# Performance work log

Hardware: AMD Instinct MI355X
Metric: run time of the kernel (lower is better)

## Reference

```python
import jax, jax.numpy as jnp
import numpy as np

B, L, E, H = 1024, 50, 256, 256
NEG = -1e9          # stands in for -inf masked_fill (exp(NEG) == 0 in fp32)
C_EXPL = 10.0       # tanh_exploration for the pointer head
N_GLIMPSES = 1


def setup_inputs() -> dict:
    key = jax.random.key(0)
    ks = jax.random.split(key, 20)
    s = 1.0 / np.sqrt(H).astype(np.float32)
    return {
        "decoder_input": jax.random.normal(ks[0], (B, E), jnp.float32),
        "embedded_inputs": jax.random.normal(ks[1], (L, B, E), jnp.float32),
        "h0": jax.random.normal(ks[2], (B, H), jnp.float32),
        "c0": jax.random.normal(ks[3], (B, H), jnp.float32),
        "context": jax.random.normal(ks[4], (L, B, H), jnp.float32),
        "init_mask": jnp.zeros((B, L), dtype=bool),
        "lstm_Wih": jax.random.normal(ks[5], (4 * H, E), jnp.float32) * s,
        "lstm_Whh": jax.random.normal(ks[6], (4 * H, H), jnp.float32) * s,
        "lstm_bih": jax.random.normal(ks[7], (4 * H,), jnp.float32) * s,
        "lstm_bhh": jax.random.normal(ks[8], (4 * H,), jnp.float32) * s,
        "gl_Wq": jax.random.normal(ks[9], (H, H), jnp.float32) * s,
        "gl_bq": jax.random.normal(ks[10], (H,), jnp.float32) * s,
        "gl_Wref": jax.random.normal(ks[11], (H, H), jnp.float32) * s,
        "gl_bref": jax.random.normal(ks[12], (H,), jnp.float32) * s,
        "gl_v": jax.random.uniform(ks[13], (H,), jnp.float32, -s, s),
        "pt_Wq": jax.random.normal(ks[14], (H, H), jnp.float32) * s,
        "pt_bq": jax.random.normal(ks[15], (H, H // H * H,)[:1] and (H,), jnp.float32) * s,
        "pt_Wref": jax.random.normal(ks[16], (H, H), jnp.float32) * s,
        "pt_bref": jax.random.normal(ks[17], (H,), jnp.float32) * s,
        "pt_v": jax.random.uniform(ks[18], (H,), jnp.float32, -s, s),
    }


def _attention(Wq, bq, Wref, bref, v, query, context, use_tanh):
    # context: [L,B,H], query: [B,H]
    e = jnp.einsum('lbh,oh->lbo', context, Wref) + bref      # conv1d(k=1) proj of ref
    q = query @ Wq.T + bq                                    # [B,H]
    u = jnp.einsum('lbh,h->bl', jnp.tanh(q[None, :, :] + e), v)
    if use_tanh:
        u = C_EXPL * jnp.tanh(u)
    return e, u


def _lstm_cell(x, h, c, Wih, Whh, bih, bhh):
    g = x @ Wih.T + bih + h @ Whh.T + bhh
    i, f, gg, o = jnp.split(g, 4, axis=1)   # torch LSTMCell gate order: i,f,g,o
    c2 = jax.nn.sigmoid(f) * c + jax.nn.sigmoid(i) * jnp.tanh(gg)
    h2 = jax.nn.sigmoid(o) * jnp.tanh(c2)
    return h2, c2


def reference(decoder_input, embedded_inputs, h0, c0, context, init_mask,
              lstm_Wih, lstm_Whh, lstm_bih, lstm_bhh,
              gl_Wq, gl_bq, gl_Wref, gl_bref, gl_v,
              pt_Wq, pt_bq, pt_Wref, pt_bref, pt_v):
    batch_idx = jnp.arange(B)

    def step(carry, t):
        h, c, mask, idxs, dec_in = carry
        # update_mask(mask, selected), skipped at step 0 (prev_idxs is None)
        safe = jnp.maximum(idxs, 0)
        m2 = mask.at[batch_idx, safe].set(True)
        m2 = m2.at[:, -1].set(jnp.where(m2.all(axis=1), False, m2[:, -1]))
        logit_mask = jnp.where(t == 0, mask, m2)
        # LSTM cell
        hy, cy = _lstm_cell(dec_in, h, c, lstm_Wih, lstm_Whh, lstm_bih, lstm_bhh)
        g_l = hy
        # glimpse attention(s) (mask_glimpses=True)
        for _ in range(N_GLIMPSES):
            e, gl = _attention(gl_Wq, gl_bq, gl_Wref, gl_bref, gl_v, g_l, context, False)
            gl = jnp.where(logit_mask, NEG, gl)
            g_l = jnp.einsum('lbh,bl->bh', e, jax.nn.softmax(gl, axis=1))
        # pointer attention (mask_logits=True)
        _, logits = _attention(pt_Wq, pt_bq, pt_Wref, pt_bref, pt_v, g_l, context, True)
        logits = jnp.where(logit_mask, NEG, logits)
        log_p = jax.nn.log_softmax(logits, axis=1)          # [B,L]
        new_idxs = jax.lax.stop_gradient(jnp.argmax(log_p, axis=1))  # greedy decode (detached)
        new_dec_in = embedded_inputs[new_idxs, batch_idx]   # gather next input [B,E]
        return (hy, cy, logit_mask, new_idxs, new_dec_in), (log_p, new_idxs)

    init = (h0, c0, init_mask, jnp.full((B,), -1, dtype=jnp.int32), decoder_input)
    _, (log_ps, sels) = jax.lax.scan(step, init, jnp.arange(L))
    # stack along time dim 1, as torch.stack(outputs, 1)
    return jnp.transpose(log_ps, (1, 0, 2)), jnp.transpose(sels, (1, 0))
```

## Files before the change

### kernel.cpp

```cpp
#include <hip/hip_runtime.h>
#include <math.h>

#define Bsz 1024
#define Lsz 50
#define Esz 256
#define Hsz 256
#define NEGV (-1e9f)

__global__ void init_kernel(const float* __restrict__ dec0,
                            float* __restrict__ dec,
                            int* __restrict__ mask)
{
    int i = blockIdx.x * 256 + threadIdx.x;
    dec[i] = dec0[i];
    if (i < Bsz * Lsz) mask[i] = 0;
}

__global__ void pack_wq(const float* __restrict__ WqGl, const float* __restrict__ WqPt,
                        float* __restrict__ WqGlP, float* __restrict__ WqPtP)
{
    int k = blockIdx.x;
    int n = threadIdx.x;
    const float* src = blockIdx.y ? WqPt : WqGl;
    float*       dst = blockIdx.y ? WqPtP : WqGlP;
    dst[((size_t)(k >> 2) * 256 + n) * 4 + (k & 3)] = src[(size_t)n * 256 + k];
}

__global__ __launch_bounds__(256) void eproj_kernel(
    const float* __restrict__ A,
    const float* __restrict__ Wgl, const float* __restrict__ bgl, float* __restrict__ Egl,
    const float* __restrict__ Wpt, const float* __restrict__ bpt, float* __restrict__ Ept)
{
    __shared__ __align__(16) float As[16][68];
    __shared__ __align__(16) float Bs[16][68];
    const int tid = threadIdx.x;
    const int tx = tid & 15, ty = tid >> 4;
    const int ml = tid >> 2;
    const int kb = (tid & 3) << 2;

    const int x = blockIdx.x;
    const int xcd = x & 7;
    const int j = x >> 3;
    const int mt = xcd * 100 + (j >> 3);
    const int sel = (j >> 2) & 1;
    const int nt = j & 3;
    const float* W    = sel ? Wpt : Wgl;
    const float* bias = sel ? bpt : bgl;
    float*       Eo   = sel ? Ept : Egl;
    const int m0 = mt * 64, n0 = nt * 64;

    float4 a4 = *(const float4*)(A + (size_t)(m0 + ml) * 256 + kb);
    float4 b4 = *(const float4*)(W + (size_t)(n0 + ml) * 256 + kb);

    float acc[4][4] = {};
    for (int k0 = 0; k0 < 256; k0 += 16) {
        As[kb+0][ml] = a4.x; As[kb+1][ml] = a4.y; As[kb+2][ml] = a4.z; As[kb+3][ml] = a4.w;
        Bs[kb+0][ml] = b4.x; Bs[kb+1][ml] = b4.y; Bs[kb+2][ml] = b4.z; Bs[kb+3][ml] = b4.w;
        __syncthreads();
        int k1 = k0 + 16;
        if (k1 < 256) {
            a4 = *(const float4*)(A + (size_t)(m0 + ml) * 256 + k1 + kb);
            b4 = *(const float4*)(W + (size_t)(n0 + ml) * 256 + k1 + kb);
        }
#pragma unroll
        for (int kk = 0; kk < 16; kk++) {
            float4 av = *(const float4*)(&As[kk][ty << 2]);
            float4 bv = *(const float4*)(&Bs[kk][tx << 2]);
            float a_[4] = {av.x, av.y, av.z, av.w};
            float b_[4] = {bv.x, bv.y, bv.z, bv.w};
#pragma unroll
            for (int i = 0; i < 4; i++)
#pragma unroll
                for (int j2 = 0; j2 < 4; j2++) acc[i][j2] = fmaf(a_[i], b_[j2], acc[i][j2]);
        }
        __syncthreads();
    }
#pragma unroll
    for (int i = 0; i < 4; i++) {
        int m = m0 + (ty << 2) + i;
        int bb = m & (Bsz - 1);
        int ll = m >> 10;
#pragma unroll
        for (int j2 = 0; j2 < 4; j2++) {
            int n = n0 + (tx << 2) + j2;
            Eo[(size_t)bb * Lsz * Hsz + (size_t)ll * Hsz + n] = acc[i][j2] + bias[n];
        }
    }
}

__global__ __launch_bounds__(256) void lstm_fused(
    const float* __restrict__ dec, const float* __restrict__ hprev,
    const float* __restrict__ cin,
    const float* __restrict__ Wih, const float* __restrict__ Whh,
    const float* __restrict__ bih, const float* __restrict__ bhh,
    float* __restrict__ hout, float* __restrict__ cout)
{
    __shared__ __align__(16) float As[16][36];
    __shared__ __align__(16) float Bs[16][68];
    const int tid = threadIdx.x;
    const int tx = tid & 15, ty = tid >> 4;
    const int mlA = tid >> 3;
    const int kbA = (tid & 7) << 1;
    const int mlB = tid >> 2;
    const int kbB = (tid & 3) << 2;
    const int m0 = blockIdx.x * 32;
    const int hh0 = blockIdx.y * 16;
    const int wrow = ((mlB >> 4) << 8) + hh0 + (mlB & 15);
    const int pcol = ((mlB & 15) << 2) + (mlB >> 4);

    float2 a2 = *(const float2*)(dec + (size_t)(m0 + mlA) * 256 + kbA);
    float4 b4 = *(const float4*)(Wih + (size_t)wrow * 256 + kbB);

    float acc[2][4] = {};
    for (int k0 = 0; k0 < 512; k0 += 16) {
        As[kbA+0][mlA] = a2.x; As[kbA+1][mlA] = a2.y;
        Bs[kbB+0][pcol] = b4.x; Bs[kbB+1][pcol] = b4.y;
        Bs[kbB+2][pcol] = b4.z; Bs[kbB+3][pcol] = b4.w;
        __syncthreads();
        int k1 = k0 + 16;
        if (k1 < 512) {
            const float* Ap = (k1 < 256) ? dec : hprev;
            const float* Wp = (k1 < 256) ? Wih : Whh;
            int kk0 = k1 & 255;
            a2 = *(const float2*)(Ap + (size_t)(m0 + mlA) * 256 + kk0 + kbA);
            b4 = *(const float4*)(Wp + (size_t)wrow * 256 + kk0 + kbB);
        }
#pragma unroll
        for (int kk = 0; kk < 16; kk++) {
            float2 av = *(const float2*)(&As[kk][ty << 1]);
            float4 bv = *(const float4*)(&Bs[kk][tx << 2]);
            acc[0][0] = fmaf(av.x, bv.x, acc[0][0]);
            acc[0][1] = fmaf(av.x, bv.y, acc[0][1]);
            acc[0][2] = fmaf(av.x, bv.z, acc[0][2]);
            acc[0][3] = fmaf(av.x, bv.w, acc[0][3]);
            acc[1][0] = fmaf(av.y, bv.x, acc[1][0]);
            acc[1][1] = fmaf(av.y, bv.y, acc[1][1]);
            acc[1][2] = fmaf(av.y, bv.z, acc[1][2]);
            acc[1][3] = fmaf(av.y, bv.w, acc[1][3]);
        }
        __syncthreads();
    }

    const int hh = hh0 + tx;
    const float bi0 = bih[hh]       + bhh[hh];
    const float bf  = bih[256 + hh] + bhh[256 + hh];
    const float bg  = bih[512 + hh] + bhh[512 + hh];
    const float bo  = bih[768 + hh] + bhh[768 + hh];
#pragma unroll
    for (int i = 0; i < 2; i++) {
        int m = m0 + (ty << 1) + i;
        float gi = acc[i][0] + bi0;
        float gf = acc[i][1] + bf;
        float gc = acc[i][2] + bg;
        float go = acc[i][3] + bo;
        float ii = 1.0f / (1.0f + expf(-gi));
        float ff = 1.0f / (1.0f + expf(-gf));
        float oo = 1.0f / (1.0f + expf(-go));
        float c2 = ff * cin[(size_t)m * 256 + hh] + ii * tanhf(gc);
        hout[(size_t)m * 256 + hh] = oo * tanhf(c2);
        cout[(size_t)m * 256 + hh] = c2;
    }
}

__global__ __launch_bounds__(256) void attn_row(
    const float* __restrict__ h,
    const float* __restrict__ WqGlP, const float* __restrict__ glbq,
    const float* __restrict__ e_gl, const float* __restrict__ glv,
    const float* __restrict__ WqPtP, const float* __restrict__ ptbq,
    const float* __restrict__ e_pt, const float* __restrict__ ptv,
    int* __restrict__ mask, float* __restrict__ out, int t,
    float* __restrict__ dec, const float* __restrict__ emb)
{
    __shared__ __align__(16) float h_s[256];
    __shared__ __align__(16) float q_s[256];
    __shared__ __align__(16) float g_s[256];
    __shared__ float u_s[64];
    __shared__ float p_s[64];
    __shared__ int sel_s;

    const int tid = threadIdx.x;
    const int lane = tid & 63, wave = tid >> 6;
    const int b = blockIdx.x;

    h_s[tid] = h[(size_t)b * 256 + tid];
    __syncthreads();

    {
        float q = glbq[tid];
        const float4* Wp = (const float4*)WqGlP;
#pragma unroll 8
        for (int k4 = 0; k4 < 64; k4++) {
            float4 w  = Wp[(size_t)k4 * 256 + tid];
            float4 hv = ((const float4*)h_s)[k4];
            q = fmaf(hv.x, w.x, q);
            q = fmaf(hv.y, w.y, q);
            q = fmaf(hv.z, w.z, q);
            q = fmaf(hv.w, w.w, q);
        }
        q_s[tid] = q;
    }
    __syncthreads();

    const float* ebg = e_gl + (size_t)b * Lsz * 256;
    {
        const float4 q4 = ((const float4*)q_s)[lane];
        const float4 v4 = ((const float4*)glv)[lane];
#pragma unroll
        for (int lp = 0; lp < 13; lp++) {
            const int l = lp * 4 + wave;
            float x = 0.0f;
            if (l < Lsz) {
                float4 e4 = *(const float4*)(ebg + (size_t)l * 256 + (lane << 2));
                x  = v4.x * tanhf(q4.x + e4.x);
                x += v4.y * tanhf(q4.y + e4.y);
                x += v4.z * tanhf(q4.z + e4.z);
                x += v4.w * tanhf(q4.w + e4.w);
            }
#pragma unroll
            for (int o = 32; o > 0; o >>= 1) x += __shfl_xor(x, o, 64);
            if (lane == 0 && l < Lsz) u_s[l] = x;
        }
    }
    __syncthreads();

    if (wave == 0) {
        const int l = lane;
        const int ml = (l < Lsz) ? mask[b * Lsz + l] : 0;
        float logit = (l < Lsz) ? (ml ? NEGV : u_s[l]) : -1e30f;
        float m = logit;
#pragma unroll
        for (int o = 32; o > 0; o >>= 1) m = fmaxf(m, __shfl_xor(m, o, 64));
        float ex = (l < Lsz) ? expf(logit - m) : 0.0f;
        float den = ex;
#pragma unroll
        for (int o = 32; o > 0; o >>= 1) den += __shfl_xor(den, o, 64);
        if (l < Lsz) p_s[l] = ex / den;
    }
    __syncthreads();

    {
        float acc = 0.0f;
        const float* ebh = ebg + tid;
#pragma unroll
        for (int l = 0; l < Lsz; l++)
            acc = fmaf(p_s[l], ebh[(size_t)l * 256], acc);
        g_s[tid] = acc;
    }
    __syncthreads();

    {
        float p = ptbq[tid];
        const float4* Wp = (const float4*)WqPtP;
#pragma unroll 8
        for (int k4 = 0; k4 < 64; k4++) {
            float4 w  = Wp[(size_t)k4 * 256 + tid];
            float4 gv = ((const float4*)g_s)[k4];
            p = fmaf(gv.x, w.x, p);
            p = fmaf(gv.y, w.y, p);
            p = fmaf(gv.z, w.z, p);
            p = fmaf(gv.w, w.w, p);
        }
        q_s[tid] = p;
    }
    __syncthreads();

    const float* ebp = e_pt + (size_t)b * Lsz * 256;
    {
        const float4 q4 = ((const float4*)q_s)[lane];
        const float4 v4 = ((const float4*)ptv)[lane];
#pragma unroll
        for (int lp = 0; lp < 13; lp++) {
            const int l = lp * 4 + wave;
            float x = 0.0f;
            if (l < Lsz) {
                float4 e4 = *(const float4*)(ebp + (size_t)l * 256 + (lane << 2));
                x  = v4.x * tanhf(q4.x + e4.x);
                x += v4.y * tanhf(q4.y + e4.y);
                x += v4.z * tanhf(q4.z + e4.z);
                x += v4.w * tanhf(q4.w + e4.w);
            }
#pragma unroll
            for (int o = 32; o > 0; o >>= 1) x += __shfl_xor(x, o, 64);
            if (lane == 0 && l < Lsz) u_s[l] = x;
        }
    }
    __syncthreads();

    if (wave == 0) {
        const int l = lane;
        const int ml = (l < Lsz) ? mask[b * Lsz + l] : 0;
        float logit;
        if (l < Lsz) {
            float u = u_s[l];
            logit = 10.0f * tanhf(u);
            if (ml) logit = NEGV;
        } else logit = -1e30f;

        float m = logit;
#pragma unroll
        for (int o = 32; o > 0; o >>= 1) m = fmaxf(m, __shfl_xor(m, o, 64));
        float ex = (l < Lsz) ? expf(logit - m) : 0.0f;
        float den = ex;
#pragma unroll
        for (int o = 32; o > 0; o >>= 1) den += __shfl_xor(den, o, 64);

        float av = logit; int ai = (l < Lsz) ? l : 63;
#pragma unroll
        for (int o = 32; o > 0; o >>= 1) {
            float ov = __shfl_xor(av, o, 64);
            int   oi = __shfl_xor(ai, o, 64);
            if (ov > av || (ov == av && oi < ai)) { av = ov; ai = oi; }
        }
        const float lse = m + logf(den);
        if (l < Lsz)
            out[(size_t)b * Lsz * Lsz + (size_t)t * Lsz + l] = logit - lse;
        if (l == 0) {
            out[(size_t)Bsz * Lsz * Lsz + (size_t)b * Lsz + t] = (float)ai;
            sel_s = ai;
        }
        int newm = ml | (l == ai);
        unsigned long long bal = __ballot(l >= Lsz ? 1 : newm);
        int all = (bal == 0xFFFFFFFFFFFFFFFFull);
        if (l < Lsz) mask[b * Lsz + l] = (all && l == Lsz - 1) ? 0 : newm;
    }
    __syncthreads();

    {
        const int s = sel_s;
        dec[(size_t)b * 256 + tid] = emb[(size_t)s * Bsz * 256 + (size_t)b * 256 + tid];
    }
}

extern "C" void kernel_launch(void* const* d_in, const int* in_sizes, int n_in,
                              void* d_out, int out_size, void* d_ws, size_t ws_size,
                              hipStream_t stream) {
    const float* decoder_input = (const float*)d_in[0];
    const float* emb           = (const float*)d_in[1];
    const float* h0            = (const float*)d_in[2];
    const float* c0            = (const float*)d_in[3];
    const float* context       = (const float*)d_in[4];
    const float* Wih    = (const float*)d_in[6];
    const float* Whh    = (const float*)d_in[7];
    const float* bih    = (const float*)d_in[8];
    const float* bhh    = (const float*)d_in[9];
    const float* glWq   = (const float*)d_in[10];
    const float* glbq   = (const float*)d_in[11];
    const float* glWref = (const float*)d_in[12];
    const float* glbref = (const float*)d_in[13];
    const float* glv    = (const float*)d_in[14];
    const float* ptWq   = (const float*)d_in[15];
    const float* ptbq   = (const float*)d_in[16];
    const float* ptWref = (const float*)d_in[17];
    const float* ptbref = (const float*)d_in[18];
    const float* ptv    = (const float*)d_in[19];

    float* out = (float*)d_out;

    float* ws    = (float*)d_ws;
    float* e_gl  = ws;
    float* e_pt  = e_gl + (size_t)Bsz * Lsz * Hsz;
    float* WqGlP = e_pt + (size_t)Bsz * Lsz * Hsz;
    float* WqPtP = WqGlP + (size_t)Hsz * Hsz;
    float* hb0   = WqPtP + (size_t)Hsz * Hsz;
    float* hb1   = hb0 + (size_t)Bsz * Hsz;
    float* cb0   = hb1 + (size_t)Bsz * Hsz;
    float* cb1   = cb0 + (size_t)Bsz * Hsz;
    float* dec   = cb1 + (size_t)Bsz * Hsz;
    int*   mask  = (int*)(dec + (size_t)Bsz * Esz);

    float* hbuf[2] = {hb0, hb1};
    float* cbuf[2] = {cb0, cb1};

    init_kernel<<<dim3(Bsz), dim3(256), 0, stream>>>(decoder_input, dec, mask);
    pack_wq<<<dim3(256, 2), dim3(256), 0, stream>>>(glWq, ptWq, WqGlP, WqPtP);

    eproj_kernel<<<dim3(6400), dim3(256), 0, stream>>>(
        context, glWref, glbref, e_gl, ptWref, ptbref, e_pt);

    for (int t = 0; t < Lsz; t++) {
        const float* hin = (t == 0) ? h0 : hbuf[(t + 1) & 1];
        const float* cin = (t == 0) ? c0 : cbuf[(t + 1) & 1];
        float* hout = hbuf[t & 1];
        float* cout = cbuf[t & 1];

        lstm_fused<<<dim3(32, 16), dim3(256), 0, stream>>>(
            dec, hin, cin, Wih, Whh, bih, bhh, hout, cout);

        attn_row<<<dim3(Bsz), dim3(256), 0, stream>>>(
            hout, WqGlP, glbq, e_gl, glv, WqPtP, ptbq, e_pt, ptv,
            mask, out, t, dec, emb);
    }
}
```

Baseline: 4.141 ms.

## Fuse decode loop into one cooperative persistent kernel with group counters

```diff
diff --git a/kernel.cpp b/kernel.cpp
--- a/kernel.cpp
+++ b/kernel.cpp
@@ -9,11 +9,13 @@
 
 __global__ void init_kernel(const float* __restrict__ dec0,
                             float* __restrict__ dec,
-                            int* __restrict__ mask)
+                            int* __restrict__ mask,
+                            int* __restrict__ cnts)
 {
     int i = blockIdx.x * 256 + threadIdx.x;
     dec[i] = dec0[i];
     if (i < Bsz * Lsz) mask[i] = 0;
+    if (i < 64) cnts[i] = 0;
 }
 
 __global__ void pack_wq(const float* __restrict__ WqGl, const float* __restrict__ WqPt,
@@ -328,6 +330,288 @@
     {
         const int s = sel_s;
         dec[(size_t)b * 256 + tid] = emb[(size_t)s * Bsz * 256 + (size_t)b * 256 + tid];
+    }
+}
+
+__global__ __launch_bounds__(256, 4) void decode_loop(
+    const float* __restrict__ h0, const float* __restrict__ c0,
+    const float* __restrict__ Wih, const float* __restrict__ Whh,
+    const float* __restrict__ bih, const float* __restrict__ bhh,
+    const float* __restrict__ WqGlP, const float* __restrict__ glbq,
+    const float* __restrict__ e_gl, const float* __restrict__ glv,
+    const float* __restrict__ WqPtP, const float* __restrict__ ptbq,
+    const float* __restrict__ e_pt, const float* __restrict__ ptv,
+    const float* __restrict__ emb,
+    float* __restrict__ hb0, float* __restrict__ hb1,
+    float* __restrict__ dec, float* __restrict__ out,
+    int* __restrict__ hcnt, int* __restrict__ deccnt)
+{
+    __shared__ __align__(16) float As[16][36];
+    __shared__ __align__(16) float Bs[16][68];
+    __shared__ __align__(16) float h_s[256];
+    __shared__ __align__(16) float q_s[256];
+    __shared__ __align__(16) float g_s[256];
+    __shared__ float u_s[64];
+    __shared__ float p_s[64];
+    __shared__ int  mask_s[64];
+    __shared__ int  sel_s;
+
+    const int tid  = threadIdx.x;
+    const int bid  = blockIdx.x;
+    const int g    = bid >> 5;
+    const int lane = tid & 63, wave = tid >> 6;
+    const bool is_lstm = (bid & 1) == 0;
+
+    const int lstm_id = bid >> 1;
+    const int tx = tid & 15, ty = tid >> 4;
+    const int mlA = tid >> 3, kbA = (tid & 7) << 1;
+    const int mlB = tid >> 2, kbB = (tid & 3) << 2;
+    const int m0  = (lstm_id >> 4) * 32;
+    const int hh0 = (lstm_id & 15) * 16;
+    const int wrow = ((mlB >> 4) << 8) + hh0 + (mlB & 15);
+    const int pcol = ((mlB & 15) << 2) + (mlB >> 4);
+    const int hh = hh0 + tx;
+
+    float creg[2] = {0.f, 0.f};
+    float bi0 = 0.f, bfv = 0.f, bgv = 0.f, bov = 0.f;
+    if (is_lstm) {
+        bi0 = bih[hh]       + bhh[hh];
+        bfv = bih[256 + hh] + bhh[256 + hh];
+        bgv = bih[512 + hh] + bhh[512 + hh];
+        bov = bih[768 + hh] + bhh[768 + hh];
+#pragma unroll
+        for (int i = 0; i < 2; i++) {
+            int m = m0 + (ty << 1) + i;
+            creg[i] = c0[(size_t)m * 256 + hh];
+        }
+    }
+    if (tid < 64) mask_s[tid] = 0;
+
+    const float* ebg = e_gl + (size_t)bid * Lsz * 256;
+    const float* ebp = e_pt + (size_t)bid * Lsz * 256;
+
+    for (int t = 0; t < Lsz; t++) {
+        float* hout = (t & 1) ? hb1 : hb0;
+
+        if (is_lstm) {
+            const float* hin = (t == 0) ? h0 : ((t & 1) ? hb0 : hb1);
+            if (t > 0) {
+                if (tid == 0) {
+                    while (__hip_atomic_load(&deccnt[g], __ATOMIC_RELAXED,
+                                             __HIP_MEMORY_SCOPE_AGENT) < 32 * t)
+                        __builtin_amdgcn_s_sleep(2);
+                    __threadfence();
+                }
+                __syncthreads();
+            }
+
+            float2 a2 = *(const float2*)(dec + (size_t)(m0 + mlA) * 256 + kbA);
+            float4 b4 = *(const float4*)(Wih + (size_t)wrow * 256 + kbB);
+
+            float acc[2][4] = {};
+            for (int k0 = 0; k0 < 512; k0 += 16) {
+                As[kbA+0][mlA] = a2.x; As[kbA+1][mlA] = a2.y;
+                Bs[kbB+0][pcol] = b4.x; Bs[kbB+1][pcol] = b4.y;
+                Bs[kbB+2][pcol] = b4.z; Bs[kbB+3][pcol] = b4.w;
+                __syncthreads();
+                int k1 = k0 + 16;
+                if (k1 < 512) {
+                    const float* Ap = (k1 < 256) ? dec : hin;
+                    const float* Wp = (k1 < 256) ? Wih : Whh;
+                    int kk0 = k1 & 255;
+                    a2 = *(const float2*)(Ap + (size_t)(m0 + mlA) * 256 + kk0 + kbA);
+                    b4 = *(const float4*)(Wp + (size_t)wrow * 256 + kk0 + kbB);
+                }
+#pragma unroll
+                for (int kk = 0; kk < 16; kk++) {
+                    float2 av = *(const float2*)(&As[kk][ty << 1]);
+                    float4 bv = *(const float4*)(&Bs[kk][tx << 2]);
+                    acc[0][0] = fmaf(av.x, bv.x, acc[0][0]);
+                    acc[0][1] = fmaf(av.x, bv.y, acc[0][1]);
+                    acc[0][2] = fmaf(av.x, bv.z, acc[0][2]);
+                    acc[0][3] = fmaf(av.x, bv.w, acc[0][3]);
+                    acc[1][0] = fmaf(av.y, bv.x, acc[1][0]);
+                    acc[1][1] = fmaf(av.y, bv.y, acc[1][1]);
+                    acc[1][2] = fmaf(av.y, bv.z, acc[1][2]);
+                    acc[1][3] = fmaf(av.y, bv.w, acc[1][3]);
+                }
+                __syncthreads();
+            }
+
+#pragma unroll
+            for (int i = 0; i < 2; i++) {
+                int m = m0 + (ty << 1) + i;
+                float gi = acc[i][0] + bi0;
+                float gf = acc[i][1] + bfv;
+                float gc = acc[i][2] + bgv;
+                float go = acc[i][3] + bov;
+                float ii = 1.0f / (1.0f + expf(-gi));
+                float ff = 1.0f / (1.0f + expf(-gf));
+                float oo = 1.0f / (1.0f + expf(-go));
+                float c2 = ff * creg[i] + ii * tanhf(gc);
+                creg[i] = c2;
+                hout[(size_t)m * 256 + hh] = oo * tanhf(c2);
+            }
+            __syncthreads();
+            if (tid == 0) { __threadfence(); atomicAdd(&hcnt[g], 1); }
+        }
+
+        if (tid == 0) {
+            while (__hip_atomic_load(&hcnt[g], __ATOMIC_RELAXED,
+                                     __HIP_MEMORY_SCOPE_AGENT) < 16 * (t + 1))
+                __builtin_amdgcn_s_sleep(2);
+            __threadfence();
+        }
+        __syncthreads();
+
+        h_s[tid] = hout[(size_t)bid * 256 + tid];
+        __syncthreads();
+
+        {
+            float q = glbq[tid];
+            const float4* Wp = (const float4*)WqGlP;
+#pragma unroll 8
+            for (int k4 = 0; k4 < 64; k4++) {
+                float4 w  = Wp[(size_t)k4 * 256 + tid];
+                float4 hv = ((const float4*)h_s)[k4];
+                q = fmaf(hv.x, w.x, q);
+                q = fmaf(hv.y, w.y, q);
+                q = fmaf(hv.z, w.z, q);
+                q = fmaf(hv.w, w.w, q);
+            }
+            q_s[tid] = q;
+        }
+        __syncthreads();
+
+        {
+            const float4 q4 = ((const float4*)q_s)[lane];
+            const float4 v4 = ((const float4*)glv)[lane];
+#pragma unroll
+            for (int lp = 0; lp < 13; lp++) {
+                const int l = lp * 4 + wave;
+                float x = 0.0f;
+                if (l < Lsz) {
+                    float4 e4 = *(const float4*)(ebg + (size_t)l * 256 + (lane << 2));
+                    x  = v4.x * tanhf(q4.x + e4.x);
+                    x += v4.y * tanhf(q4.y + e4.y);
+                    x += v4.z * tanhf(q4.z + e4.z);
+                    x += v4.w * tanhf(q4.w + e4.w);
+                }
+#pragma unroll
+                for (int o = 32; o > 0; o >>= 1) x += __shfl_xor(x, o, 64);
+                if (lane == 0 && l < Lsz) u_s[l] = x;
+            }
+        }
+        __syncthreads();
+
+        if (wave == 0) {
+            const int l = lane;
+            const int ml = (l < Lsz) ? mask_s[l] : 0;
+            float logit = (l < Lsz) ? (ml ? NEGV : u_s[l]) : -1e30f;
+            float m = logit;
+#pragma unroll
+            for (int o = 32; o > 0; o >>= 1) m = fmaxf(m, __shfl_xor(m, o, 64));
+            float ex = (l < Lsz) ? expf(logit - m) : 0.0f;
+            float den = ex;
+#pragma unroll
+            for (int o = 32; o > 0; o >>= 1) den += __shfl_xor(den, o, 64);
+            if (l < Lsz) p_s[l] = ex / den;
+        }
+        __syncthreads();
+
+        {
+            float acc = 0.0f;
+            const float* ebh = ebg + tid;
+#pragma unroll
+            for (int l = 0; l < Lsz; l++)
+                acc = fmaf(p_s[l], ebh[(size_t)l * 256], acc);
+            g_s[tid] = acc;
+        }
+        __syncthreads();
+
+        {
+            float p = ptbq[tid];
+            const float4* Wp = (const float4*)WqPtP;
+#pragma unroll 8
+            for (int k4 = 0; k4 < 64; k4++) {
+                float4 w  = Wp[(size_t)k4 * 256 + tid];
+                float4 gv = ((const float4*)g_s)[k4];
+                p = fmaf(gv.x, w.x, p);
+                p = fmaf(gv.y, w.y, p);
+                p = fmaf(gv.z, w.z, p);
+                p = fmaf(gv.w, w.w, p);
+            }
+            q_s[tid] = p;
+        }
+        __syncthreads();
+
+        {
+            const float4 q4 = ((const float4*)q_s)[lane];
+            const float4 v4 = ((const float4*)ptv)[lane];
+#pragma unroll
+            for (int lp = 0; lp < 13; lp++) {
+                const int l = lp * 4 + wave;
+                float x = 0.0f;
+                if (l < Lsz) {
+                    float4 e4 = *(const float4*)(ebp + (size_t)l * 256 + (lane << 2));
+                    x  = v4.x * tanhf(q4.x + e4.x);
+                    x += v4.y * tanhf(q4.y + e4.y);
+                    x += v4.z * tanhf(q4.z + e4.z);
+                    x += v4.w * tanhf(q4.w + e4.w);
+                }
+#pragma unroll
+                for (int o = 32; o > 0; o >>= 1) x += __shfl_xor(x, o, 64);
+                if (lane == 0 && l < Lsz) u_s[l] = x;
+            }
+        }
+        __syncthreads();
+
+        if (wave == 0) {
+            const int l = lane;
+            const int ml = (l < Lsz) ? mask_s[l] : 0;
+            float logit;
+            if (l < Lsz) {
+                float u = u_s[l];
+                logit = 10.0f * tanhf(u);
+                if (ml) logit = NEGV;
+            } else logit = -1e30f;
+
+            float m = logit;
+#pragma unroll
+            for (int o = 32; o > 0; o >>= 1) m = fmaxf(m, __shfl_xor(m, o, 64));
+            float ex = (l < Lsz) ? expf(logit - m) : 0.0f;
+            float den = ex;
+#pragma unroll
+            for (int o = 32; o > 0; o >>= 1) den += __shfl_xor(den, o, 64);
+
+            float av = logit; int ai = (l < Lsz) ? l : 63;
+#pragma unroll
+            for (int o = 32; o > 0; o >>= 1) {
+                float ov = __shfl_xor(av, o, 64);
+                int   oi = __shfl_xor(ai, o, 64);
+                if (ov > av || (ov == av && oi < ai)) { av = ov; ai = oi; }
+            }
+            const float lse = m + logf(den);
+            if (l < Lsz)
+                out[(size_t)bid * Lsz * Lsz + (size_t)t * Lsz + l] = logit - lse;
+            if (l == 0) {
+                out[(size_t)Bsz * Lsz * Lsz + (size_t)bid * Lsz + t] = (float)ai;
+                sel_s = ai;
+            }
+            int newm = ml | (l == ai);
+            unsigned long long bal = __ballot(l >= Lsz ? 1 : newm);
+            int all = (bal == 0xFFFFFFFFFFFFFFFFull);
+            if (l < Lsz) mask_s[l] = (all && l == Lsz - 1) ? 0 : newm;
+        }
+        __syncthreads();
+
+        {
+            const int s = sel_s;
+            dec[(size_t)bid * 256 + tid] =
+                emb[(size_t)s * Bsz * 256 + (size_t)bid * 256 + tid];
+        }
+        __syncthreads();
+        if (tid == 0) { __threadfence(); atomicAdd(&deccnt[g], 1); }
     }
 }
 
@@ -367,27 +651,42 @@
     float* cb1   = cb0 + (size_t)Bsz * Hsz;
     float* dec   = cb1 + (size_t)Bsz * Hsz;
     int*   mask  = (int*)(dec + (size_t)Bsz * Esz);
-
-    float* hbuf[2] = {hb0, hb1};
-    float* cbuf[2] = {cb0, cb1};
-
-    init_kernel<<<dim3(Bsz), dim3(256), 0, stream>>>(decoder_input, dec, mask);
+    int*   cnts  = mask + (size_t)Bsz * Lsz;
+    int*   hcnt   = cnts;
+    int*   deccnt = cnts + 32;
+
+    init_kernel<<<dim3(Bsz), dim3(256), 0, stream>>>(decoder_input, dec, mask, cnts);
     pack_wq<<<dim3(256, 2), dim3(256), 0, stream>>>(glWq, ptWq, WqGlP, WqPtP);
 
     eproj_kernel<<<dim3(6400), dim3(256), 0, stream>>>(
         context, glWref, glbref, e_gl, ptWref, ptbref, e_pt);
 
-    for (int t = 0; t < Lsz; t++) {
-        const float* hin = (t == 0) ? h0 : hbuf[(t + 1) & 1];
-        const float* cin = (t == 0) ? c0 : cbuf[(t + 1) & 1];
-        float* hout = hbuf[t & 1];
-        float* cout = cbuf[t & 1];
-
-        lstm_fused<<<dim3(32, 16), dim3(256), 0, stream>>>(
-            dec, hin, cin, Wih, Whh, bih, bhh, hout, cout);
-
-        attn_row<<<dim3(Bsz), dim3(256), 0, stream>>>(
-            hout, WqGlP, glbq, e_gl, glv, WqPtP, ptbq, e_pt, ptv,
-            mask, out, t, dec, emb);
+    void* kargs[] = {
+        (void*)&h0, (void*)&c0, (void*)&Wih, (void*)&Whh,
+        (void*)&bih, (void*)&bhh, (void*)&WqGlP, (void*)&glbq,
+        (void*)&e_gl, (void*)&glv, (void*)&WqPtP, (void*)&ptbq,
+        (void*)&e_pt, (void*)&ptv, (void*)&emb,
+        (void*)&hb0, (void*)&hb1, (void*)&dec, (void*)&out,
+        (void*)&hcnt, (void*)&deccnt
+    };
+    hipError_t err = hipLaunchCooperativeKernel(
+        (const void*)decode_loop, dim3(Bsz), dim3(256), kargs, 0, stream);
+
+    if (err != hipSuccess) {
+        float* hbuf[2] = {hb0, hb1};
+        float* cbuf[2] = {cb0, cb1};
+        for (int t = 0; t < Lsz; t++) {
+            const float* hin = (t == 0) ? h0 : hbuf[(t + 1) & 1];
+            const float* cin = (t == 0) ? c0 : cbuf[(t + 1) & 1];
+            float* hout = hbuf[t & 1];
+            float* cout = cbuf[t & 1];
+
+            lstm_fused<<<dim3(32, 16), dim3(256), 0, stream>>>(
+                dec, hin, cin, Wih, Whh, bih, bhh, hout, cout);
+
+            attn_row<<<dim3(Bsz), dim3(256), 0, stream>>>(
+                hout, WqGlP, glbq, e_gl, glv, WqPtP, ptbq, e_pt, ptv,
+                mask, out, t, dec, emb);
+        }
     }
 }
```

Result: slower. 14.26 ms (+244.3%).

## Process two batch rows per attention block and fold setup kernels into eproj

Applied to the files above, without the earlier changes.

```diff
diff --git a/kernel.cpp b/kernel.cpp
--- a/kernel.cpp
+++ b/kernel.cpp
@@ -7,33 +7,27 @@
 #define Hsz 256
 #define NEGV (-1e9f)
 
-__global__ void init_kernel(const float* __restrict__ dec0,
-                            float* __restrict__ dec,
-                            int* __restrict__ mask)
-{
-    int i = blockIdx.x * 256 + threadIdx.x;
-    dec[i] = dec0[i];
-    if (i < Bsz * Lsz) mask[i] = 0;
-}
-
-__global__ void pack_wq(const float* __restrict__ WqGl, const float* __restrict__ WqPt,
-                        float* __restrict__ WqGlP, float* __restrict__ WqPtP)
-{
-    int k = blockIdx.x;
-    int n = threadIdx.x;
-    const float* src = blockIdx.y ? WqPt : WqGl;
-    float*       dst = blockIdx.y ? WqPtP : WqGlP;
-    dst[((size_t)(k >> 2) * 256 + n) * 4 + (k & 3)] = src[(size_t)n * 256 + k];
-}
-
-__global__ __launch_bounds__(256) void eproj_kernel(
+__global__ __launch_bounds__(256) void eproj_pack(
     const float* __restrict__ A,
     const float* __restrict__ Wgl, const float* __restrict__ bgl, float* __restrict__ Egl,
-    const float* __restrict__ Wpt, const float* __restrict__ bpt, float* __restrict__ Ept)
+    const float* __restrict__ Wpt, const float* __restrict__ bpt, float* __restrict__ Ept,
+    const float* __restrict__ WqGl, const float* __restrict__ WqPt,
+    float* __restrict__ WqGlP, float* __restrict__ WqPtP)
 {
     __shared__ __align__(16) float As[16][68];
     __shared__ __align__(16) float Bs[16][68];
     const int tid = threadIdx.x;
+
+    if (blockIdx.x >= 6400) {
+        const int p = blockIdx.x - 6400;
+        const int sel = p >> 8;
+        const int k = p & 255;
+        const float* src = sel ? WqPt : WqGl;
+        float*       dst = sel ? WqPtP : WqGlP;
+        dst[((size_t)(k >> 2) * 256 + tid) * 4 + (k & 3)] = src[(size_t)tid * 256 + k];
+        return;
+    }
+
     const int tx = tid & 15, ty = tid >> 4;
     const int ml = tid >> 2;
     const int kb = (tid & 3) << 2;
@@ -162,7 +156,7 @@
     }
 }
 
-__global__ __launch_bounds__(256) void attn_row(
+__global__ __launch_bounds__(256) void attn_row2(
     const float* __restrict__ h,
     const float* __restrict__ WqGlP, const float* __restrict__ glbq,
     const float* __restrict__ e_gl, const float* __restrict__ glv,
@@ -171,62 +165,70 @@
     int* __restrict__ mask, float* __restrict__ out, int t,
     float* __restrict__ dec, const float* __restrict__ emb)
 {
-    __shared__ __align__(16) float h_s[256];
-    __shared__ __align__(16) float q_s[256];
-    __shared__ __align__(16) float g_s[256];
-    __shared__ float u_s[64];
-    __shared__ float p_s[64];
-    __shared__ int sel_s;
+    __shared__ __align__(16) float h_s[2][256];
+    __shared__ __align__(16) float q_s[2][256];
+    __shared__ __align__(16) float g_s[2][256];
+    __shared__ float u_s[2][64];
+    __shared__ float p_s[2][64];
+    __shared__ int  sel_s[2];
 
     const int tid = threadIdx.x;
     const int lane = tid & 63, wave = tid >> 6;
-    const int b = blockIdx.x;
-
-    h_s[tid] = h[(size_t)b * 256 + tid];
-    __syncthreads();
-
-    {
-        float q = glbq[tid];
+    const int r0 = blockIdx.x * 2, r1 = r0 + 1;
+
+    h_s[0][tid] = h[(size_t)r0 * 256 + tid];
+    h_s[1][tid] = h[(size_t)r1 * 256 + tid];
+    __syncthreads();
+
+    {
+        float q0 = glbq[tid], q1 = q0;
         const float4* Wp = (const float4*)WqGlP;
 #pragma unroll 8
         for (int k4 = 0; k4 < 64; k4++) {
-            float4 w  = Wp[(size_t)k4 * 256 + tid];
-            float4 hv = ((const float4*)h_s)[k4];
-            q = fmaf(hv.x, w.x, q);
-            q = fmaf(hv.y, w.y, q);
-            q = fmaf(hv.z, w.z, q);
-            q = fmaf(hv.w, w.w, q);
-        }
-        q_s[tid] = q;
-    }
-    __syncthreads();
-
-    const float* ebg = e_gl + (size_t)b * Lsz * 256;
-    {
-        const float4 q4 = ((const float4*)q_s)[lane];
+            float4 w   = Wp[(size_t)k4 * 256 + tid];
+            float4 h0v = ((const float4*)h_s[0])[k4];
+            float4 h1v = ((const float4*)h_s[1])[k4];
+            q0 = fmaf(h0v.x, w.x, q0);
+            q0 = fmaf(h0v.y, w.y, q0);
+            q0 = fmaf(h0v.z, w.z, q0);
+            q0 = fmaf(h0v.w, w.w, q0);
+            q1 = fmaf(h1v.x, w.x, q1);
+            q1 = fmaf(h1v.y, w.y, q1);
+            q1 = fmaf(h1v.z, w.z, q1);
+            q1 = fmaf(h1v.w, w.w, q1);
+        }
+        q_s[0][tid] = q0; q_s[1][tid] = q1;
+    }
+    __syncthreads();
+
+    const int urow = wave >> 1, w2 = wave & 1;
+    const int rgu = r0 + urow;
+    const float* ebgu = e_gl + (size_t)rgu * Lsz * 256;
+    const float* ebpu = e_pt + (size_t)rgu * Lsz * 256;
+
+    {
+        const float4 q4 = ((const float4*)q_s[urow])[lane];
         const float4 v4 = ((const float4*)glv)[lane];
 #pragma unroll
-        for (int lp = 0; lp < 13; lp++) {
-            const int l = lp * 4 + wave;
-            float x = 0.0f;
-            if (l < Lsz) {
-                float4 e4 = *(const float4*)(ebg + (size_t)l * 256 + (lane << 2));
-                x  = v4.x * tanhf(q4.x + e4.x);
-                x += v4.y * tanhf(q4.y + e4.y);
-                x += v4.z * tanhf(q4.z + e4.z);
-                x += v4.w * tanhf(q4.w + e4.w);
-            }
+        for (int lp = 0; lp < 25; lp++) {
+            const int l = lp * 2 + w2;
+            float4 e4 = *(const float4*)(ebgu + (size_t)l * 256 + (lane << 2));
+            float x  = v4.x * tanhf(q4.x + e4.x);
+            x += v4.y * tanhf(q4.y + e4.y);
+            x += v4.z * tanhf(q4.z + e4.z);
+            x += v4.w * tanhf(q4.w + e4.w);
 #pragma unroll
             for (int o = 32; o > 0; o >>= 1) x += __shfl_xor(x, o, 64);
-            if (lane == 0 && l < Lsz) u_s[l] = x;
-        }
-    }
-    __syncthreads();
-
-    if (wave == 0) {
+            if (lane == 0) u_s[urow][l] = x;
+        }
+    }
+    __syncthreads();
+
+    if (wave < 2) {
+        const int row = wave, rg = r0 + row;
         const int l = lane;
-        const int ml = (l < Lsz) ? mask[b * Lsz + l] : 0;
-        float logit = (l < Lsz) ? (ml ? NEGV : u_s[l]) : -1e30f;
+        const int ml = (l < Lsz && t > 0) ? mask[rg * Lsz + l] : 0;
+        float logit = (l < Lsz) ? (ml ? NEGV : u_s[row][l]) : -1e30f;
         float m = logit;
 #pragma unroll
         for (int o = 32; o > 0; o >>= 1) m = fmaxf(m, __shfl_xor(m, o, 64));
@@ -234,64 +236,69 @@
         float den = ex;
 #pragma unroll
         for (int o = 32; o > 0; o >>= 1) den += __shfl_xor(den, o, 64);
-        if (l < Lsz) p_s[l] = ex / den;
-    }
-    __syncthreads();
-
-    {
-        float acc = 0.0f;
-        const float* ebh = ebg + tid;
-#pragma unroll
-        for (int l = 0; l < Lsz; l++)
-            acc = fmaf(p_s[l], ebh[(size_t)l * 256], acc);
-        g_s[tid] = acc;
-    }
-    __syncthreads();
-
-    {
-        float p = ptbq[tid];
+        if (l < Lsz) p_s[row][l] = ex / den;
+    }
+    __syncthreads();
+
+    {
+        float a0 = 0.0f, a1 = 0.0f;
+        const float* eb0 = e_gl + (size_t)r0 * Lsz * 256 + tid;
+        const float* eb1 = e_gl + (size_t)r1 * Lsz * 256 + tid;
+#pragma unroll
+        for (int l = 0; l < Lsz; l++) {
+            a0 = fmaf(p_s[0][l], eb0[(size_t)l * 256], a0);
+            a1 = fmaf(p_s[1][l], eb1[(size_t)l * 256], a1);
+        }
+        g_s[0][tid] = a0; g_s[1][tid] = a1;
+    }
+    __syncthreads();
+
+    {
+        float p0 = ptbq[tid], p1 = p0;
         const float4* Wp = (const float4*)WqPtP;
 #pragma unroll 8
         for (int k4 = 0; k4 < 64; k4++) {
-            float4 w  = Wp[(size_t)k4 * 256 + tid];
-            float4 gv = ((const float4*)g_s)[k4];
-            p = fmaf(gv.x, w.x, p);
-            p = fmaf(gv.y, w.y, p);
-            p = fmaf(gv.z, w.z, p);
-            p = fmaf(gv.w, w.w, p);
-        }
-        q_s[tid] = p;
-    }
-    __syncthreads();
-
-    const float* ebp = e_pt + (size_t)b * Lsz * 256;
-    {
-        const float4 q4 = ((const float4*)q_s)[lane];
+            float4 w   = Wp[(size_t)k4 * 256 + tid];
+            float4 g0v = ((const float4*)g_s[0])[k4];
+            float4 g1v = ((const float4*)g_s[1])[k4];
+            p0 = fmaf(g0v.x, w.x, p0);
+            p0 = fmaf(g0v.y, w.y, p0);
+            p0 = fmaf(g0v.z, w.z, p0);
+            p0 = fmaf(g0v.w, w.w, p0);
+            p1 = fmaf(g1v.x, w.x, p1);
+            p1 = fmaf(g1v.y, w.y, p1);
+            p1 = fmaf(g1v.z, w.z, p1);
+            p1 = fmaf(g1v.w, w.w, p1);
+        }
+        q_s[0][tid] = p0; q_s[1][tid] = p1;
+    }
+    __syncthreads();
+
+    {
+        const float4 q4 = ((const float4*)q_s[urow])[lane];
         const float4 v4 = ((const float4*)ptv)[lane];
 #pragma unroll
-        for (int lp = 0; lp < 13; lp++) {
-            const int l = lp * 4 + wave;
-            float x = 0.0f;
-            if (l < Lsz) {
-                float4 e4 = *(const float4*)(ebp + (size_t)l * 256 + (lane << 2));
-                x  = v4.x * tanhf(q4.x + e4.x);
-                x += v4.y * tanhf(q4.y + e4.y);
-                x += v4.z * tanhf(q4.z + e4.z);
-                x += v4.w * tanhf(q4.w + e4.w);
-            }
+        for (int lp = 0; lp < 25; lp++) {
+            const int l = lp * 2 + w2;
+            float4 e4 = *(const float4*)(ebpu + (size_t)l * 256 + (lane << 2));
+            float x  = v4.x * tanhf(q4.x + e4.x);
+            x += v4.y * tanhf(q4.y + e4.y);
+            x += v4.z * tanhf(q4.z + e4.z);
+            x += v4.w * tanhf(q4.w + e4.w);
 #pragma unroll
             for (int o = 32; o > 0; o >>= 1) x += __shfl_xor(x, o, 64);
-            if (lane == 0 && l < Lsz) u_s[l] = x;
-        }
-    }
-    __syncthreads();
-
-    if (wave == 0) {
+            if (lane == 0) u_s[urow][l] = x;
+        }
+    }
+    __syncthreads();
+
+    if (wave < 2) {
+        const int row = wave, rg = r0 + row;
         const int l = lane;
-        const int ml = (l < Lsz) ? mask[b * Lsz + l] : 0;
+        const int ml = (l < Lsz && t > 0) ? mask[rg * Lsz + l] : 0;
         float logit;
         if (l < Lsz) {
-            float u = u_s[l];
+            float u = u_s[row][l];
             logit = 10.0f * tanhf(u);
             if (ml) logit = NEGV;
         } else logit = -1e30f;
@@ -313,21 +320,23 @@
         }
         const float lse = m + logf(den);
         if (l < Lsz)
-            out[(size_t)b * Lsz * Lsz + (size_t)t * Lsz + l] = logit - lse;
+            out[(size_t)rg * Lsz * Lsz + (size_t)t * Lsz + l] = logit - lse;
         if (l == 0) {
-            out[(size_t)Bsz * Lsz * Lsz + (size_t)b * Lsz + t] = (float)ai;
-            sel_s = ai;
+            out[(size_t)Bsz * Lsz * Lsz + (size_t)rg * Lsz + t] = (float)ai;
+            sel_s[row] = ai;
         }
         int newm = ml | (l == ai);
         unsigned long long bal = __ballot(l >= Lsz ? 1 : newm);
         int all = (bal == 0xFFFFFFFFFFFFFFFFull);
-        if (l < Lsz) mask[b * Lsz + l] = (all && l == Lsz - 1) ? 0 : newm;
-    }
-    __syncthreads();
-
-    {
-        const int s = sel_s;
-        dec[(size_t)b * 256 + tid] = emb[(size_t)s * Bsz * 256 + (size_t)b * 256 + tid];
+        if (l < Lsz) mask[rg * Lsz + l] = (all && l == Lsz - 1) ? 0 : newm;
+    }
+    __syncthreads();
+
+    {
+        dec[(size_t)r0 * 256 + tid] =
+            emb[(size_t)sel_s[0] * Bsz * 256 + (size_t)r0 * 256 + tid];
+        dec[(size_t)r1 * 256 + tid] =
+            emb[(size_t)sel_s[1] * Bsz * 256 + (size_t)r1 * 256 + tid];
     }
 }
 
@@ -371,22 +380,21 @@
     float* hbuf[2] = {hb0, hb1};
     float* cbuf[2] = {cb0, cb1};
 
-    init_kernel<<<dim3(Bsz), dim3(256), 0, stream>>>(decoder_input, dec, mask);
-    pack_wq<<<dim3(256, 2), dim3(256), 0, stream>>>(glWq, ptWq, WqGlP, WqPtP);
-
-    eproj_kernel<<<dim3(6400), dim3(256), 0, stream>>>(
-        context, glWref, glbref, e_gl, ptWref, ptbref, e_pt);
+    eproj_pack<<<dim3(6912), dim3(256), 0, stream>>>(
+        context, glWref, glbref, e_gl, ptWref, ptbref, e_pt,
+        glWq, ptWq, WqGlP, WqPtP);
 
     for (int t = 0; t < Lsz; t++) {
+        const float* Ain = (t == 0) ? decoder_input : dec;
         const float* hin = (t == 0) ? h0 : hbuf[(t + 1) & 1];
         const float* cin = (t == 0) ? c0 : cbuf[(t + 1) & 1];
         float* hout = hbuf[t & 1];
         float* cout = cbuf[t & 1];
 
         lstm_fused<<<dim3(32, 16), dim3(256), 0, stream>>>(
-            dec, hin, cin, Wih, Whh, bih, bhh, hout, cout);
-
-        attn_row<<<dim3(Bsz), dim3(256), 0, stream>>>(
+            Ain, hin, cin, Wih, Whh, bih, bhh, hout, cout);
+
+        attn_row2<<<dim3(512), dim3(256), 0, stream>>>(
             hout, WqGlP, glbq, e_gl, glv, WqPtP, ptbq, e_pt, ptv,
             mask, out, t, dec, emb);
     }
```

Measured after the change: 6.328 ms. 52.8% more time.
